# Kernel optimization log

Hardware: AMD Instinct MI355X
Metric: run time of the kernel (lower is better)

The kernel has to match this reference:

```python
import jax, jax.numpy as jnp
import numpy as np

B = 32          # number of graphs
N_PER = 1000    # num_nodes per graph (CDSQN.num_nodes)
TOTAL = B * N_PER
E = 512000      # edges (avg degree 16)
F_IN = 128      # node_feat_dim
HID = 128       # hidden_dim (= GNN embedding_dim)
D = 64          # dsf_hidden_dim
NH = 3          # num_heads
EPS = 1e-6


def setup_inputs() -> dict:
    key = jax.random.key(0)
    ks = jax.random.split(key, 12)
    x = jax.random.normal(ks[0], (TOTAL, F_IN), jnp.float32)
    edge_index = jax.random.randint(ks[1], (2, E), 0, TOTAL, dtype=jnp.int64)
    batch_index = jnp.repeat(jnp.arange(B, dtype=jnp.int64), N_PER)
    actions = (jax.random.uniform(ks[2], (B, N_PER)) < 0.1).astype(jnp.float32)

    def lin(k, fan_in, fan_out):
        s = 1.0 / np.sqrt(fan_in)
        return jax.random.uniform(k, (fan_in, fan_out), jnp.float32, -s, s)

    Wc1 = lin(ks[3], F_IN, HID); bc1 = jnp.zeros((HID,), jnp.float32)
    Wc2 = lin(ks[4], HID, HID);  bc2 = jnp.zeros((HID,), jnp.float32)
    Wc3 = lin(ks[5], HID, HID);  bc3 = jnp.zeros((HID,), jnp.float32)
    Wg1 = lin(ks[6], HID, NH * N_PER * D); bg1 = jnp.full((NH * N_PER * D,), 0.1, jnp.float32)
    Wg2 = lin(ks[7], HID, NH * D * D);     bg2 = jnp.full((NH * D * D,), 0.1, jnp.float32)
    Wg3 = lin(ks[8], HID, NH * D);         bg3 = jnp.full((NH * D,), 0.1, jnp.float32)
    return dict(x=x, edge_index=edge_index, batch_index=batch_index, actions=actions,
                Wc1=Wc1, bc1=bc1, Wc2=Wc2, bc2=bc2, Wc3=Wc3, bc3=bc3,
                Wg1=Wg1, bg1=bg1, Wg2=Wg2, bg2=bg2, Wg3=Wg3, bg3=bg3)


def _gcn(h, W, b, src, dst, norm):
    # PyG GCNConv: h' = D^-1/2 (A+I) D^-1/2 (h W) + b ; src/dst include self loops
    h = h @ W
    msgs = h[src] * norm[:, None]            # [E+TOTAL, out]
    return jax.ops.segment_sum(msgs, dst, num_segments=TOTAL) + b


def reference(x, edge_index, batch_index, actions,
              Wc1, bc1, Wc2, bc2, Wc3, bc3,
              Wg1, bg1, Wg2, bg2, Wg3, bg3):
    loops = jnp.arange(TOTAL, dtype=edge_index.dtype)
    src = jnp.concatenate([edge_index[0], loops])
    dst = jnp.concatenate([edge_index[1], loops])
    deg = jax.ops.segment_sum(jnp.ones(src.shape[0], x.dtype), dst, num_segments=TOTAL)
    dinv = jnp.where(deg > 0, jax.lax.rsqrt(deg), 0.0)
    norm = dinv[src] * dinv[dst]

    h = jax.nn.relu(_gcn(x, Wc1, bc1, src, dst, norm))
    h = jax.nn.relu(_gcn(h, Wc2, bc2, src, dst, norm))
    h = _gcn(h, Wc3, bc3, src, dst, norm)

    # global_mean_pool
    cnt = jax.ops.segment_sum(jnp.ones(TOTAL, x.dtype), batch_index, num_segments=B)
    h_g = jax.ops.segment_sum(h, batch_index, num_segments=B) / cnt[:, None]  # [B, HID]

    # hypernetwork weights
    w1 = jax.nn.softplus((h_g @ Wg1 + bg1).reshape(B, NH, N_PER, D))
    w2 = jax.nn.softplus((h_g @ Wg2 + bg2).reshape(B, NH, D, D))
    w3 = jax.nn.softplus((h_g @ Wg3 + bg3).reshape(B, NH, D))

    # compute_q (2D actions branch)
    h1 = jnp.einsum('bn,bhnd->bhd', actions, w1)
    h1 = jnp.sqrt(jnp.clip(h1, 0.0) + EPS)           # SafeSqrt
    h2 = jnp.einsum('bhd,bhde->bhe', h1, w2)
    h2 = jnp.log1p(jnp.clip(h2, 0.0))                # SafeLog: log(1+clamp(x,0))
    out_heads = jnp.einsum('bhd,bhd->bh', h2, w3)    # [B, NH]
    return jnp.min(out_heads, axis=-1)               # [B]
```

## Files before the change

kernel.cpp:

```cpp
#include <hip/hip_runtime.h>
#include <hip/hip_bf16.h>
#include <math.h>

#define NB 32
#define N_PER 1000
#define TOTALN 32000
#define NE 512000
#define HID 128
#define Dh 64
#define NH 3
#define EPSV 1e-6f
#define PCH 25
#define W1CH 250

typedef __attribute__((ext_vector_type(8))) short bf16x8;
typedef __attribute__((ext_vector_type(4))) float f32x4;

__device__ __forceinline__ float softplusf(float x) {
    return fmaxf(x, 0.0f) + log1pf(expf(-fabsf(x)));
}
__device__ __forceinline__ unsigned short f2b(float f) {
    __hip_bfloat16 h = __float2bfloat16(f);
    return __builtin_bit_cast(unsigned short, h);
}
__device__ __forceinline__ float b2f(unsigned short u) {
    unsigned int x = ((unsigned int)u) << 16;
    return __builtin_bit_cast(float, x);
}

__global__ __launch_bounds__(256) void k_init_deg(float* deg) {
    int i = blockIdx.x * 256 + threadIdx.x;
    if (i < TOTALN) deg[i] = 1.0f;
}

__global__ __launch_bounds__(256) void k_deg(const int* __restrict__ ei, float* deg) {
    int e = blockIdx.x * 256 + threadIdx.x;
    if (e < NE) atomicAdd(&deg[ei[NE + e]], 1.0f);
}

__global__ __launch_bounds__(256) void k_prep(float* __restrict__ d, int* __restrict__ cnt) {
    int i = blockIdx.x * 256 + threadIdx.x;
    if (i < TOTALN) {
        float v = d[i];
        cnt[i] = (int)v - 1;
        d[i] = rsqrtf(v);
    }
}

__global__ __launch_bounds__(256) void k_scan_block(const int* __restrict__ cnt,
                                                    int* __restrict__ rowptr,
                                                    int* __restrict__ bsum) {
    __shared__ int sh[256];
    int t = threadIdx.x;
    int i = blockIdx.x * 256 + t;
    int v = cnt[i];
    sh[t] = v;
    __syncthreads();
    for (int off = 1; off < 256; off <<= 1) {
        int add = (t >= off) ? sh[t - off] : 0;
        __syncthreads();
        sh[t] += add;
        __syncthreads();
    }
    rowptr[i] = sh[t] - v;
    if (t == 255) bsum[blockIdx.x] = sh[255];
}

__global__ void k_scan_tot(int* __restrict__ bsum) {
    if (threadIdx.x == 0) {
        int run = 0;
        for (int i = 0; i < 125; ++i) { int t = bsum[i]; bsum[i] = run; run += t; }
    }
}

__global__ __launch_bounds__(256) void k_scan_add(int* __restrict__ rowptr,
                                                  const int* __restrict__ bsum,
                                                  int* __restrict__ cursor) {
    int i = blockIdx.x * 256 + threadIdx.x;
    int v = rowptr[i] + bsum[blockIdx.x];
    rowptr[i] = v;
    cursor[i] = v;
    if (i == 0) rowptr[TOTALN] = NE;
}

__global__ __launch_bounds__(256) void k_fill(const int* __restrict__ ei,
                                              const float* __restrict__ dinv,
                                              int* __restrict__ cursor,
                                              int* __restrict__ csr_src,
                                              float* __restrict__ csr_w) {
    int e = blockIdx.x * 256 + threadIdx.x;
    if (e < NE) {
        int s = ei[e], d = ei[NE + e];
        int pos = atomicAdd(&cursor[d], 1);
        csr_src[pos] = s;
        csr_w[pos] = dinv[s] * dinv[d];
    }
}

__global__ __launch_bounds__(256) void k_wcvt(const float* __restrict__ W,
                                              unsigned short* __restrict__ Wt) {
    int i = blockIdx.x * 256 + threadIdx.x;
    int k = i >> 7, c = i & 127;
    Wt[c * 128 + k] = f2b(W[i]);
}

template<int INF32>
__global__ __launch_bounds__(256) void k_mm(const void* __restrict__ Xv,
                                            const unsigned short* __restrict__ Wt,
                                            unsigned short* __restrict__ Y) {
    int tid = threadIdx.x;
    int wv = tid >> 6, l = tid & 63;
    int row0 = blockIdx.x * 64 + wv * 16;
    int r = l & 15, kc = l >> 4;
    bf16x8 a[4];
    if (INF32) {
        const float* X = (const float*)Xv;
#pragma unroll
        for (int ks = 0; ks < 4; ++ks) {
            const float* p = X + (long)(row0 + r) * 128 + ks * 32 + kc * 8;
            float4 f0 = *(const float4*)p;
            float4 f1 = *(const float4*)(p + 4);
            bf16x8 t;
            t[0] = (short)f2b(f0.x); t[1] = (short)f2b(f0.y);
            t[2] = (short)f2b(f0.z); t[3] = (short)f2b(f0.w);
            t[4] = (short)f2b(f1.x); t[5] = (short)f2b(f1.y);
            t[6] = (short)f2b(f1.z); t[7] = (short)f2b(f1.w);
            a[ks] = t;
        }
    } else {
        const unsigned short* X = (const unsigned short*)Xv;
#pragma unroll
        for (int ks = 0; ks < 4; ++ks)
            a[ks] = *(const bf16x8*)(X + (long)(row0 + r) * 128 + ks * 32 + kc * 8);
    }
    f32x4 acc[8];
#pragma unroll
    for (int nt = 0; nt < 8; ++nt) acc[nt] = (f32x4){0.f, 0.f, 0.f, 0.f};
#pragma unroll
    for (int ks = 0; ks < 4; ++ks) {
#pragma unroll
        for (int nt = 0; nt < 8; ++nt) {
            bf16x8 b = *(const bf16x8*)(Wt + (nt * 16 + r) * 128 + ks * 32 + kc * 8);
            acc[nt] = __builtin_amdgcn_mfma_f32_16x16x32_bf16(a[ks], b, acc[nt], 0, 0, 0);
        }
    }
#pragma unroll
    for (int nt = 0; nt < 8; ++nt)
#pragma unroll
        for (int j = 0; j < 4; ++j)
            Y[(long)(row0 + kc * 4 + j) * 128 + nt * 16 + r] = f2b(acc[nt][j]);
}

template<int MODE>
__global__ __launch_bounds__(256) void k_gather(const unsigned short* __restrict__ feat,
                                                unsigned short* __restrict__ out,
                                                const int* __restrict__ rowptr,
                                                const int* __restrict__ csr_src,
                                                const float* __restrict__ csr_w,
                                                const float* __restrict__ dinv,
                                                const float* __restrict__ bias) {
    int wid = threadIdx.x >> 6, lane = threadIdx.x & 63;
    int v = blockIdx.x * 4 + wid;
    const unsigned int* f2 = (const unsigned int*)feat;
    float dv = dinv[v];
    unsigned int sv = f2[v * 64 + lane];
    float acc0 = b2f((unsigned short)(sv & 0xffff)) * dv * dv;
    float acc1 = b2f((unsigned short)(sv >> 16)) * dv * dv;
    int e = rowptr[v], e1 = rowptr[v + 1];
    for (; e + 4 <= e1; e += 4) {
        int s0 = csr_src[e], s1 = csr_src[e + 1], s2 = csr_src[e + 2], s3 = csr_src[e + 3];
        float w0 = csr_w[e], w1 = csr_w[e + 1], w2 = csr_w[e + 2], w3 = csr_w[e + 3];
        unsigned int u0 = f2[s0 * 64 + lane];
        unsigned int u1 = f2[s1 * 64 + lane];
        unsigned int u2 = f2[s2 * 64 + lane];
        unsigned int u3 = f2[s3 * 64 + lane];
        acc0 += b2f((unsigned short)(u0 & 0xffff)) * w0 + b2f((unsigned short)(u1 & 0xffff)) * w1
              + b2f((unsigned short)(u2 & 0xffff)) * w2 + b2f((unsigned short)(u3 & 0xffff)) * w3;
        acc1 += b2f((unsigned short)(u0 >> 16)) * w0 + b2f((unsigned short)(u1 >> 16)) * w1
              + b2f((unsigned short)(u2 >> 16)) * w2 + b2f((unsigned short)(u3 >> 16)) * w3;
    }
    for (; e < e1; ++e) {
        int s = csr_src[e];
        float w = csr_w[e];
        unsigned int u = f2[s * 64 + lane];
        acc0 += b2f((unsigned short)(u & 0xffff)) * w;
        acc1 += b2f((unsigned short)(u >> 16)) * w;
    }
    if (MODE == 0) {
        int c = lane * 2;
        acc0 = fmaxf(acc0 + bias[c], 0.f);
        acc1 = fmaxf(acc1 + bias[c + 1], 0.f);
    }
    ((unsigned int*)out)[v * 64 + lane] =
        (unsigned int)f2b(acc0) | ((unsigned int)f2b(acc1) << 16);
}

__global__ __launch_bounds__(256) void k_pool1(const unsigned short* __restrict__ A,
                                               float* __restrict__ pp) {
    __shared__ float sh[256];
    int b = blockIdx.x / PCH, ch = blockIdx.x % PCH;
    int c = threadIdx.x & 127, half = threadIdx.x >> 7;
    float acc = 0.f;
    int n0 = ch * 40;
#pragma unroll 4
    for (int j = half; j < 40; j += 2)
        acc += b2f(A[(long)(b * N_PER + n0 + j) * 128 + c]);
    sh[threadIdx.x] = acc;
    __syncthreads();
    if (threadIdx.x < 128)
        pp[blockIdx.x * 128 + c] = sh[c] + sh[128 + c];
}

__global__ __launch_bounds__(256) void k_pool2(const float* __restrict__ pp,
                                               const float* __restrict__ bias,
                                               float* __restrict__ hg,
                                               float* __restrict__ hgT) {
    int i = blockIdx.x * 256 + threadIdx.x;
    if (i >= NB * 128) return;
    int b = i >> 7, c = i & 127;
    float s = 0.f;
#pragma unroll
    for (int ch = 0; ch < PCH; ++ch)
        s += pp[(b * PCH + ch) * 128 + c];
    float v = s * (1.0f / N_PER) + bias[c];
    hg[i] = v;
    hgT[c * NB + b] = v;
}

__global__ __launch_bounds__(512) void k_w1(const float* __restrict__ hgT,
                                            const float* __restrict__ Wg1,
                                            const float* __restrict__ bg1,
                                            const float* __restrict__ actions,
                                            float* __restrict__ p1) {
    __shared__ float red[4][32][64];
    int h = blockIdx.x / W1CH, chunk = blockIdx.x % W1CH;
    int tid = threadIdx.x;
    int wv = tid >> 6, d = tid & 63;
    int khalf = wv & 1, nsub = wv >> 1;
    int n = chunk * 4 + nsub;
    const long KS = (long)NH * N_PER * Dh;
    long col = (long)(h * N_PER + n) * Dh + d;
    const float* Wp = Wg1 + col;
    int k0 = __builtin_amdgcn_readfirstlane(khalf * 64);
    float acc[32];
#pragma unroll
    for (int b = 0; b < 32; ++b) acc[b] = 0.f;
    float4 wc;
    wc.x = Wp[(long)(k0 + 0) * KS];
    wc.y = Wp[(long)(k0 + 1) * KS];
    wc.z = Wp[(long)(k0 + 2) * KS];
    wc.w = Wp[(long)(k0 + 3) * KS];
    for (int kk = 0; kk < 64; kk += 4) {
        int k = k0 + kk;
        float4 wn = make_float4(0.f, 0.f, 0.f, 0.f);
        if (kk + 4 < 64) {
            wn.x = Wp[(long)(k + 4) * KS];
            wn.y = Wp[(long)(k + 5) * KS];
            wn.z = Wp[(long)(k + 6) * KS];
            wn.w = Wp[(long)(k + 7) * KS];
        }
#pragma unroll
        for (int kq = 0; kq < 4; ++kq) {
            float w = (kq == 0) ? wc.x : (kq == 1) ? wc.y : (kq == 2) ? wc.z : wc.w;
            const float* hp = hgT + (k + kq) * NB;
#pragma unroll
            for (int b = 0; b < 32; ++b)
                acc[b] = fmaf(hp[b], w, acc[b]);
        }
        wc = wn;
    }
    if (khalf == 0) {
#pragma unroll
        for (int b = 0; b < 32; ++b) red[nsub][b][d] = acc[b];
    }
    __syncthreads();
    if (khalf == 1) {
#pragma unroll
        for (int b = 0; b < 32; ++b) red[nsub][b][d] += acc[b];
    }
    __syncthreads();
    if (khalf == 0) {
        float bgv = bg1[col];
#pragma unroll
        for (int b = 0; b < 32; ++b)
            red[nsub][b][d] = actions[b * N_PER + n] * softplusf(red[nsub][b][d] + bgv);
    }
    __syncthreads();
    const float* rf = &red[0][0][0];
    float* po = p1 + (long)(chunk * NH + h) * 2048;
#pragma unroll
    for (int j = 0; j < 4; ++j) {
        int o = j * 512 + tid;
        po[o] = rf[o] + rf[2048 + o] + rf[4096 + o] + rf[6144 + o];
    }
}

__global__ __launch_bounds__(256) void k_red1(const float* __restrict__ p1,
                                              float* __restrict__ h1) {
    __shared__ float sh[4][64];
    int b = blockIdx.x / 3, h = blockIdx.x % 3;
    int part = threadIdx.x >> 6, d = threadIdx.x & 63;
    float s = 0.f;
    for (int ch = part; ch < W1CH; ch += 4)
        s += p1[(long)(ch * 3 + h) * 2048 + b * 64 + d];
    if (part) sh[part][d] = s;
    __syncthreads();
    if (part == 0)
        h1[(b * 3 + h) * 64 + d] = sqrtf(fmaxf(s + sh[1][d] + sh[2][d] + sh[3][d], 0.f) + EPSV);
}

__global__ __launch_bounds__(256) void k_w2(const float* __restrict__ hg,
                                            const float* __restrict__ Wg2,
                                            const float* __restrict__ bg2,
                                            const float* __restrict__ h1,
                                            float* __restrict__ p2) {
    __shared__ float hgs[32][128];
    __shared__ float wt[128][64];
    __shared__ float h1s[32];
    int hd = blockIdx.x;
    int tid = threadIdx.x;
    for (int i = 0; i < 16; ++i) {
        int idx = tid + i * 256;
        hgs[idx >> 7][idx & 127] = hg[idx];
    }
    long base = (long)hd * 64;
    for (int i = 0; i < 32; ++i) {
        int idx = tid + i * 256;
        wt[idx >> 6][idx & 63] = Wg2[(long)(idx >> 6) * (NH * Dh * Dh) + base + (idx & 63)];
    }
    int h = hd >> 6, d = hd & 63;
    if (tid < 32) h1s[tid] = h1[tid * (NH * Dh) + h * Dh + d];
    __syncthreads();
    int e = tid & 63, bq = tid >> 6;
    float bgv = bg2[base + e];
    float dot[8];
#pragma unroll
    for (int bi = 0; bi < 8; ++bi) dot[bi] = 0.f;
    for (int k = 0; k < 128; ++k) {
        float w = wt[k][e];
#pragma unroll
        for (int bi = 0; bi < 8; ++bi)
            dot[bi] += hgs[bq * 8 + bi][k] * w;
    }
    float* po = p2 + (long)hd * (32 * 64);
#pragma unroll
    for (int bi = 0; bi < 8; ++bi) {
        int b = bq * 8 + bi;
        po[b * 64 + e] = softplusf(dot[bi] + bgv) * h1s[b];
    }
}

__global__ __launch_bounds__(256) void k_red2(const float* __restrict__ p2,
                                              float* __restrict__ h2) {
    int o = blockIdx.x * 256 + threadIdx.x;
    if (o >= 32 * 192) return;
    int bh = o >> 6;
    int h = bh % 3, b = bh / 3;
    int e = o & 63;
    float s = 0.f;
    for (int d = 0; d < 64; ++d)
        s += p2[(h * 64 + d) * 2048 + b * 64 + e];
    h2[o] = log1pf(fmaxf(s, 0.f));
}

__global__ __launch_bounds__(192) void k_out(const float* __restrict__ hg,
                                             const float* __restrict__ Wg3,
                                             const float* __restrict__ bg3,
                                             const float* __restrict__ h2,
                                             float* __restrict__ out) {
    __shared__ float hgb[128];
    __shared__ float hres[NH];
    int b = blockIdx.x, tid = threadIdx.x;
    if (tid < 128) hgb[tid] = hg[b * 128 + tid];
    __syncthreads();
    int h = tid / 64, e = tid & 63;
    int c = h * 64 + e;
    float dot = 0.f;
    for (int k = 0; k < 128; ++k)
        dot += hgb[k] * Wg3[k * (NH * Dh) + c];
    float v = softplusf(dot + bg3[c]) * h2[b * 192 + c];
    for (int off = 32; off; off >>= 1)
        v += __shfl_down(v, off, 64);
    if (e == 0) hres[h] = v;
    __syncthreads();
    if (tid == 0) out[b] = fminf(fminf(hres[0], hres[1]), hres[2]);
}

extern "C" void kernel_launch(void* const* d_in, const int* in_sizes, int n_in,
                              void* d_out, int out_size, void* d_ws, size_t ws_size,
                              hipStream_t stream) {
    const float* x   = (const float*)d_in[0];
    const int*   ei  = (const int*)d_in[1];
    const float* act = (const float*)d_in[3];
    const float* Wc1 = (const float*)d_in[4];
    const float* bc1 = (const float*)d_in[5];
    const float* Wc2 = (const float*)d_in[6];
    const float* bc2 = (const float*)d_in[7];
    const float* Wc3 = (const float*)d_in[8];
    const float* bc3 = (const float*)d_in[9];
    const float* Wg1 = (const float*)d_in[10];
    const float* bg1 = (const float*)d_in[11];
    const float* Wg2 = (const float*)d_in[12];
    const float* bg2 = (const float*)d_in[13];
    const float* Wg3 = (const float*)d_in[14];
    const float* bg3 = (const float*)d_in[15];
    float* out = (float*)d_out;

    float* ws   = (float*)d_ws;
    float* dinv = ws;
    float* bufA = dinv + TOTALN;
    float* bufB = bufA + (long)TOTALN * 128;
    float* hg   = bufB + (long)TOTALN * 128;
    float* h1   = hg + 32 * 128;
    float* h2   = h1 + 32 * 192;
    float* csr_w = h2 + 32 * 192;
    float* pp   = csr_w + NE;
    float* hgT  = pp + NB * PCH * 128;
    int* cnt    = (int*)(hgT + 128 * NB);
    int* rowptr = cnt + TOTALN;
    int* cursor = rowptr + TOTALN + 4;
    int* bsum   = cursor + TOTALN;
    int* csr_src= bsum + 128;
    unsigned short* Wt = (unsigned short*)(csr_src + NE);
    unsigned short* fA = (unsigned short*)bufA;
    unsigned short* fB = (unsigned short*)bufB;
    float* p1   = bufB;
    float* p2   = bufA;

    k_init_deg<<<(TOTALN + 255) / 256, 256, 0, stream>>>(dinv);
    k_deg<<<NE / 256, 256, 0, stream>>>(ei, dinv);
    k_prep<<<(TOTALN + 255) / 256, 256, 0, stream>>>(dinv, cnt);
    k_scan_block<<<125, 256, 0, stream>>>(cnt, rowptr, bsum);
    k_scan_tot<<<1, 64, 0, stream>>>(bsum);
    k_scan_add<<<125, 256, 0, stream>>>(rowptr, bsum, cursor);
    k_fill<<<NE / 256, 256, 0, stream>>>(ei, dinv, cursor, csr_src, csr_w);

    k_wcvt<<<64, 256, 0, stream>>>(Wc1, Wt);
    k_mm<1><<<500, 256, 0, stream>>>(x, Wt, fB);
    k_gather<0><<<TOTALN / 4, 256, 0, stream>>>(fB, fA, rowptr, csr_src, csr_w, dinv, bc1);
    k_wcvt<<<64, 256, 0, stream>>>(Wc2, Wt);
    k_mm<0><<<500, 256, 0, stream>>>(fA, Wt, fB);
    k_gather<0><<<TOTALN / 4, 256, 0, stream>>>(fB, fA, rowptr, csr_src, csr_w, dinv, bc2);
    k_wcvt<<<64, 256, 0, stream>>>(Wc3, Wt);
    k_mm<0><<<500, 256, 0, stream>>>(fA, Wt, fB);
    k_gather<1><<<TOTALN / 4, 256, 0, stream>>>(fB, fA, rowptr, csr_src, csr_w, dinv, nullptr);
    k_pool1<<<NB * PCH, 256, 0, stream>>>(fA, pp);
    k_pool2<<<(NB * 128 + 255) / 256, 256, 0, stream>>>(pp, bc3, hg, hgT);

    k_w1<<<NH * W1CH, 512, 0, stream>>>(hgT, Wg1, bg1, act, p1);
    k_red1<<<96, 256, 0, stream>>>(p1, h1);
    k_w2<<<NH * Dh, 256, 0, stream>>>(hg, Wg2, bg2, h1, p2);
    k_red2<<<24, 256, 0, stream>>>(p2, h2);
    k_out<<<NB, 192, 0, stream>>>(hg, Wg3, bg3, h2, out);
}
```

Measured before the change: 293.1 us.

## Compute hypernetwork w1 GEMM with bf16 MFMA instead of scalar FMAs

Rewrites k_w1 so the 32x128 by 128x64-per-node product runs on 16x16x32 bf16 MFMA instructions. The pooled graph embedding is stored in bf16 by k_pool2, and Wg1 values are converted on the fly. Each of the 4 waves now owns one node and spans the full K, which removes the K-split reduction, and blocks shrink to 256 threads with a padded shared buffer. The kernel is dominated by streaming Wg1 (about 98 MB), so the gain depends on whether compute or the strided scalar loads were the bottleneck. It also adds bf16 rounding error to the hypernetwork weights.

```diff
diff --git a/kernel.cpp b/kernel.cpp
--- a/kernel.cpp
+++ b/kernel.cpp
@@ -214,7 +214,8 @@
 __global__ __launch_bounds__(256) void k_pool2(const float* __restrict__ pp,
                                                const float* __restrict__ bias,
                                                float* __restrict__ hg,
-                                               float* __restrict__ hgT) {
+                                               float* __restrict__ hgT,
+                                               unsigned short* __restrict__ hgB) {
     int i = blockIdx.x * 256 + threadIdx.x;
     if (i >= NB * 128) return;
     int b = i >> 7, c = i & 127;
@@ -225,73 +226,96 @@
     float v = s * (1.0f / N_PER) + bias[c];
     hg[i] = v;
     hgT[c * NB + b] = v;
-}
-
-__global__ __launch_bounds__(512) void k_w1(const float* __restrict__ hgT,
+    hgB[i] = f2b(v);
+}
+
+__global__ __launch_bounds__(256) void k_w1(const unsigned short* __restrict__ hgB,
                                             const float* __restrict__ Wg1,
                                             const float* __restrict__ bg1,
                                             const float* __restrict__ actions,
                                             float* __restrict__ p1) {
-    __shared__ float red[4][32][64];
+    __shared__ float red[32][65];
     int h = blockIdx.x / W1CH, chunk = blockIdx.x % W1CH;
     int tid = threadIdx.x;
-    int wv = tid >> 6, d = tid & 63;
-    int khalf = wv & 1, nsub = wv >> 1;
-    int n = chunk * 4 + nsub;
+    int wv = tid >> 6, l = tid & 63;
+    int r = l & 15, kc = l >> 4;
+    int n = chunk * 4 + wv;
     const long KS = (long)NH * N_PER * Dh;
-    long col = (long)(h * N_PER + n) * Dh + d;
-    const float* Wp = Wg1 + col;
-    int k0 = __builtin_amdgcn_readfirstlane(khalf * 64);
-    float acc[32];
-#pragma unroll
-    for (int b = 0; b < 32; ++b) acc[b] = 0.f;
-    float4 wc;
-    wc.x = Wp[(long)(k0 + 0) * KS];
-    wc.y = Wp[(long)(k0 + 1) * KS];
-    wc.z = Wp[(long)(k0 + 2) * KS];
-    wc.w = Wp[(long)(k0 + 3) * KS];
-    for (int kk = 0; kk < 64; kk += 4) {
-        int k = k0 + kk;
-        float4 wn = make_float4(0.f, 0.f, 0.f, 0.f);
-        if (kk + 4 < 64) {
-            wn.x = Wp[(long)(k + 4) * KS];
-            wn.y = Wp[(long)(k + 5) * KS];
-            wn.z = Wp[(long)(k + 6) * KS];
-            wn.w = Wp[(long)(k + 7) * KS];
+    long colbase = (long)h * (N_PER * Dh) + (long)n * Dh;
+    bf16x8 a[2][4];
+#pragma unroll
+    for (int mt = 0; mt < 2; ++mt)
+#pragma unroll
+        for (int ks = 0; ks < 4; ++ks)
+            a[mt][ks] = *(const bf16x8*)(hgB + (mt * 16 + r) * 128 + ks * 32 + kc * 8);
+    f32x4 acc[2][4];
+#pragma unroll
+    for (int mt = 0; mt < 2; ++mt)
+#pragma unroll
+        for (int ct = 0; ct < 4; ++ct) acc[mt][ct] = (f32x4){0.f, 0.f, 0.f, 0.f};
+#pragma unroll
+    for (int ct = 0; ct < 4; ++ct) {
+        const float* Wp = Wg1 + colbase + ct * 16 + r;
+#pragma unroll
+        for (int ks = 0; ks < 4; ++ks) {
+            int kb = ks * 32 + kc * 8;
+            float f0 = Wp[(long)(kb + 0) * KS];
+            float f1 = Wp[(long)(kb + 1) * KS];
+            float f2v = Wp[(long)(kb + 2) * KS];
+            float f3 = Wp[(long)(kb + 3) * KS];
+            float f4 = Wp[(long)(kb + 4) * KS];
+            float f5 = Wp[(long)(kb + 5) * KS];
+            float f6 = Wp[(long)(kb + 6) * KS];
+            float f7 = Wp[(long)(kb + 7) * KS];
+            bf16x8 bb;
+            bb[0] = (short)f2b(f0); bb[1] = (short)f2b(f1);
+            bb[2] = (short)f2b(f2v); bb[3] = (short)f2b(f3);
+            bb[4] = (short)f2b(f4); bb[5] = (short)f2b(f5);
+            bb[6] = (short)f2b(f6); bb[7] = (short)f2b(f7);
+            acc[0][ct] = __builtin_amdgcn_mfma_f32_16x16x32_bf16(a[0][ks], bb, acc[0][ct], 0, 0, 0);
+            acc[1][ct] = __builtin_amdgcn_mfma_f32_16x16x32_bf16(a[1][ks], bb, acc[1][ct], 0, 0, 0);
         }
-#pragma unroll
-        for (int kq = 0; kq < 4; ++kq) {
-            float w = (kq == 0) ? wc.x : (kq == 1) ? wc.y : (kq == 2) ? wc.z : wc.w;
-            const float* hp = hgT + (k + kq) * NB;
-#pragma unroll
-            for (int b = 0; b < 32; ++b)
-                acc[b] = fmaf(hp[b], w, acc[b]);
+    }
+    float actv[2][4];
+#pragma unroll
+    for (int mt = 0; mt < 2; ++mt)
+#pragma unroll
+        for (int j = 0; j < 4; ++j)
+            actv[mt][j] = actions[(mt * 16 + kc * 4 + j) * N_PER + n];
+    float bgv[4];
+#pragma unroll
+    for (int ct = 0; ct < 4; ++ct)
+        bgv[ct] = bg1[colbase + ct * 16 + r];
+    float sp[2][4][4];
+#pragma unroll
+    for (int mt = 0; mt < 2; ++mt)
+#pragma unroll
+        for (int ct = 0; ct < 4; ++ct)
+#pragma unroll
+            for (int j = 0; j < 4; ++j)
+                sp[mt][ct][j] = softplusf(acc[mt][ct][j] + bgv[ct]) * actv[mt][j];
+#pragma unroll
+    for (int ph = 0; ph < 4; ++ph) {
+        if (wv == ph) {
+#pragma unroll
+            for (int mt = 0; mt < 2; ++mt)
+#pragma unroll
+                for (int ct = 0; ct < 4; ++ct)
+#pragma unroll
+                    for (int j = 0; j < 4; ++j) {
+                        int b = mt * 16 + kc * 4 + j;
+                        int d = ct * 16 + r;
+                        if (ph == 0) red[b][d] = sp[mt][ct][j];
+                        else red[b][d] += sp[mt][ct][j];
+                    }
         }
-        wc = wn;
-    }
-    if (khalf == 0) {
-#pragma unroll
-        for (int b = 0; b < 32; ++b) red[nsub][b][d] = acc[b];
-    }
-    __syncthreads();
-    if (khalf == 1) {
-#pragma unroll
-        for (int b = 0; b < 32; ++b) red[nsub][b][d] += acc[b];
-    }
-    __syncthreads();
-    if (khalf == 0) {
-        float bgv = bg1[col];
-#pragma unroll
-        for (int b = 0; b < 32; ++b)
-            red[nsub][b][d] = actions[b * N_PER + n] * softplusf(red[nsub][b][d] + bgv);
-    }
-    __syncthreads();
-    const float* rf = &red[0][0][0];
+        __syncthreads();
+    }
     float* po = p1 + (long)(chunk * NH + h) * 2048;
 #pragma unroll
-    for (int j = 0; j < 4; ++j) {
-        int o = j * 512 + tid;
-        po[o] = rf[o] + rf[2048 + o] + rf[4096 + o] + rf[6144 + o];
+    for (int j2 = 0; j2 < 8; ++j2) {
+        int o = j2 * 256 + tid;
+        po[o] = red[o >> 6][o & 63];
     }
 }
 
@@ -416,7 +440,8 @@
     float* csr_w = h2 + 32 * 192;
     float* pp   = csr_w + NE;
     float* hgT  = pp + NB * PCH * 128;
-    int* cnt    = (int*)(hgT + 128 * NB);
+    unsigned short* hgB = (unsigned short*)(hgT + 128 * NB);
+    int* cnt    = (int*)(hgB + 4096);
     int* rowptr = cnt + TOTALN;
     int* cursor = rowptr + TOTALN + 4;
     int* bsum   = cursor + TOTALN;
@@ -445,9 +470,9 @@
     k_mm<0><<<500, 256, 0, stream>>>(fA, Wt, fB);
     k_gather<1><<<TOTALN / 4, 256, 0, stream>>>(fB, fA, rowptr, csr_src, csr_w, dinv, nullptr);
     k_pool1<<<NB * PCH, 256, 0, stream>>>(fA, pp);
-    k_pool2<<<(NB * 128 + 255) / 256, 256, 0, stream>>>(pp, bc3, hg, hgT);
-
-    k_w1<<<NH * W1CH, 512, 0, stream>>>(hgT, Wg1, bg1, act, p1);
+    k_pool2<<<(NB * 128 + 255) / 256, 256, 0, stream>>>(pp, bc3, hg, hgT, hgB);
+
+    k_w1<<<NH * W1CH, 256, 0, stream>>>(hgB, Wg1, bg1, act, p1);
     k_red1<<<96, 256, 0, stream>>>(p1, h1);
     k_w2<<<NH * Dh, 256, 0, stream>>>(hg, Wg2, bg2, h1, p2);
     k_red2<<<24, 256, 0, stream>>>(p2, h2);
```

Result: faster. 284.2 us (-3.0%).
